# Kernel optimization log

Measured on AMD Instinct MI355X. Metric: run time of the kernel, lower is better.

## Reference

```python
import jax, jax.numpy as jnp
import numpy as np

NUM_BASIS = 10
CUTOFF = 1.0
SQRT3 = 3.0 ** 0.5
SMOOTH_C = 1.14136 * float(np.exp(2.0))  # e3nn smooth_finite constant


def soft_unit_step(x):
    # e3nn soft_unit_step: exp(-1/x) for x>0 else 0 (nan-safe for grads)
    xs = jnp.where(x > 0, x, 1.0)
    return jnp.where(x > 0, jnp.exp(-1.0 / xs), 0.0)


def smooth_finite_embed(length):
    # soft_one_hot_linspace(start=0, end=cutoff, number=NUM_BASIS,
    #                       basis='smooth_finite', cutoff=True), then * sqrt(NUM_BASIS)
    values = jnp.linspace(0.0, CUTOFF, NUM_BASIS + 2)
    step = values[1] - values[0]
    values = values[1:-1]                      # [NUM_BASIS]
    diff = (length[:, None] - values) / step   # [E, NUM_BASIS]
    f = SMOOTH_C * soft_unit_step(diff + 1.0) * soft_unit_step(1.0 - diff)
    return f * (NUM_BASIS ** 0.5)


def sh_lmax2_norm(vec):
    # e3nn o3.spherical_harmonics(lmax=2, normalize=True, normalization='norm')
    r = jnp.linalg.norm(vec, axis=-1, keepdims=True)
    u = vec / jnp.where(r > 0, r, 1.0)
    x, y, z = u[:, 0], u[:, 1], u[:, 2]
    sh0 = jnp.ones_like(x)                       # l=0
    sh2_0 = SQRT3 * x * z                        # l=2 block ('norm' normalized)
    sh2_1 = SQRT3 * x * y
    sh2_2 = y * y - 0.5 * (x * x + z * z)
    sh2_3 = SQRT3 * y * z
    sh2_4 = (SQRT3 / 2.0) * (z * z - x * x)
    return jnp.stack([sh0, x, y, z, sh2_0, sh2_1, sh2_2, sh2_3, sh2_4], axis=-1)


def setup_inputs() -> dict:
    key = jax.random.key(0)
    k1, k2, k3, k4 = jax.random.split(key, 4)
    pos = jax.random.uniform(k1, (100000, 3), dtype=jnp.float32)
    query_pos = jax.random.uniform(k2, (8, 1250, 3), dtype=jnp.float32)
    # Surrogate for torch_cluster.radius(x, y, r=1.2*cutoff): fixed-size edge list
    edge_src = jax.random.randint(k3, (4000000,), 0, 10000)   # indexes flattened queries
    edge_dst = jax.random.randint(k4, (4000000,), 0, 100000)  # indexes points
    return {"pos": pos, "query_pos": query_pos, "edge_src": edge_src, "edge_dst": edge_dst}


def reference(pos, query_pos, edge_src, edge_dst):
    y = query_pos.reshape(-1, 3)                 # [Nt*Ny, 3]
    edge_vec = y[edge_src] - pos[edge_dst]       # [E, 3] irregular gather
    edge_length = jnp.linalg.norm(edge_vec, axis=-1)
    edge_length_embedded = smooth_finite_embed(edge_length)  # [E, 10]
    edge_sh = sh_lmax2_norm(edge_vec)                         # [E, 9]
    return edge_sh, edge_length_embedded
```

## Files before the change

kernel.cpp:

```cpp
#include <hip/hip_runtime.h>


#define SQRT3F 1.7320508075688772f
#define EMB_K 26.6692997f
#define TPB 256
#define EPB 256
#define NSH4 (EPB * 9 / 4)
#define NEM4 (EPB * 10 / 4)

typedef float floatx4 __attribute__((ext_vector_type(4)));

__global__ __launch_bounds__(256) void pad_kernel(
    const float* __restrict__ pos, const float* __restrict__ qpos,
    float4* __restrict__ pos4, float4* __restrict__ qpos4,
    int npos, int nq)
{
    int i = blockIdx.x * blockDim.x + threadIdx.x;
    if (i < npos)
        pos4[i] = make_float4(pos[3 * i + 0], pos[3 * i + 1], pos[3 * i + 2], 0.f);
    if (i < nq)
        qpos4[i] = make_float4(qpos[3 * i + 0], qpos[3 * i + 1], qpos[3 * i + 2], 0.f);
}

__device__ __forceinline__ void compute_edge(
    float ax, float ay, float az, float bx, float by, float bz,
    float* __restrict__ sh, float2* __restrict__ em2)
{
    float vx = ax - bx, vy = ay - by, vz = az - bz;
    float r2 = vx * vx + vy * vy + vz * vz;
    float r = sqrtf(r2);
    float inv = (r > 0.f) ? (1.f / r) : 1.f;
    float x = vx * inv, y = vy * inv, z = vz * inv;

    sh[0] = 1.f;
    sh[1] = x;
    sh[2] = y;
    sh[3] = z;
    sh[4] = SQRT3F * x * z;
    sh[5] = SQRT3F * x * y;
    sh[6] = y * y - 0.5f * (x * x + z * z);
    sh[7] = SQRT3F * y * z;
    sh[8] = 0.5f * SQRT3F * (z * z - x * x);

#pragma unroll
    for (int j = 0; j < 5; ++j) em2[j] = make_float2(0.f, 0.f);

    float t = r * 11.f;
    int k = (int)t;
    float* e = (float*)em2;
#pragma unroll
    for (int m = 0; m < 2; ++m) {
        int j = k - 1 + m;
        float a = t - (float)j;
        float b = (float)(j + 2) - t;
        if (j >= 0 && j < 10 && a > 0.f && b > 0.f)
            e[j] = EMB_K * __expf(-(__frcp_rn(a) + __frcp_rn(b)));
    }
}

template <bool PAD>
__global__ __launch_bounds__(256, 8) void qsh_kernel(
    const float* __restrict__ pos,
    const float* __restrict__ qpos,
    const float4* __restrict__ pos4,
    const float4* __restrict__ qpos4,
    const int* __restrict__ esrc,
    const int* __restrict__ edst,
    float* __restrict__ out_sh,
    float* __restrict__ out_emb,
    int n)
{
    __shared__ __align__(16) float sh_lds[EPB * 9];
    __shared__ __align__(16) float emb_lds[EPB * 10];

    const int tid = threadIdx.x;
    const int base = blockIdx.x * EPB;
    const int count = min(EPB, n - base);

    if (tid < count) {
        int e = base + tid;
        int s = __builtin_nontemporal_load(esrc + e);
        int d = __builtin_nontemporal_load(edst + e);
        float ax, ay, az, bx, by, bz;
        if (PAD) {
            float4 q = qpos4[s];
            float4 p = pos4[d];
            ax = q.x; ay = q.y; az = q.z;
            bx = p.x; by = p.y; bz = p.z;
        } else {
            ax = qpos[3 * s + 0]; ay = qpos[3 * s + 1]; az = qpos[3 * s + 2];
            bx = pos[3 * d + 0];  by = pos[3 * d + 1];  bz = pos[3 * d + 2];
        }
        compute_edge(ax, ay, az, bx, by, bz,
                     sh_lds + tid * 9, (float2*)(emb_lds + tid * 10));
    }
    __syncthreads();

    floatx4* osh4 = (floatx4*)(out_sh + (size_t)base * 9);
    floatx4* oem4 = (floatx4*)(out_emb + (size_t)base * 10);
    const floatx4* shv = (const floatx4*)sh_lds;
    const floatx4* emv = (const floatx4*)emb_lds;

    if (count == EPB) {
#pragma unroll
        for (int k = 0; k < 3; ++k) {
            int i4 = k * TPB + tid;
            if (i4 < NSH4)
                __builtin_nontemporal_store(shv[i4], osh4 + i4);
        }
#pragma unroll
        for (int k = 0; k < 3; ++k) {
            int i4 = k * TPB + tid;
            if (i4 < NEM4)
                __builtin_nontemporal_store(emv[i4], oem4 + i4);
        }
    } else {
        float* osh = out_sh + (size_t)base * 9;
        float* oem = out_emb + (size_t)base * 10;
        int nsh = count * 9;
        for (int idx = tid; idx < nsh; idx += TPB)
            __builtin_nontemporal_store(sh_lds[idx], osh + idx);
        int nem = count * 10;
        for (int idx = tid; idx < nem; idx += TPB)
            __builtin_nontemporal_store(emb_lds[idx], oem + idx);
    }
}

extern "C" void kernel_launch(void* const* d_in, const int* in_sizes, int n_in,
                              void* d_out, int out_size, void* d_ws, size_t ws_size,
                              hipStream_t stream) {
    const float* pos  = (const float*)d_in[0];
    const float* qpos = (const float*)d_in[1];
    const int* esrc = (const int*)d_in[2];
    const int* edst = (const int*)d_in[3];
    int npos = in_sizes[0] / 3;
    int nq   = in_sizes[1] / 3;
    int n    = in_sizes[2];

    float* out_sh  = (float*)d_out;
    float* out_emb = out_sh + (size_t)n * 9;

    int grid = (n + EPB - 1) / EPB;

    size_t need = ((size_t)npos + (size_t)nq) * sizeof(float4);
    if (ws_size >= need) {
        float4* pos4  = (float4*)d_ws;
        float4* qpos4 = pos4 + npos;
        int pgrid = (max(npos, nq) + TPB - 1) / TPB;
        pad_kernel<<<pgrid, TPB, 0, stream>>>(pos, qpos, pos4, qpos4, npos, nq);
        qsh_kernel<true><<<grid, TPB, 0, stream>>>(
            pos, qpos, pos4, qpos4, esrc, edst, out_sh, out_emb, n);
    } else {
        qsh_kernel<false><<<grid, TPB, 0, stream>>>(
            pos, qpos, nullptr, nullptr, esrc, edst, out_sh, out_emb, n);
    }
}
```

Before: 362.6 us.

## Stage query positions in LDS and software-pipeline a persistent edge loop

Converts the one-block-per-chunk launch into a persistent grid of 1024 blocks that walk edge chunks in a grid-stride loop. Each block copies the full query-position array (hardcoded to 30000 floats) into LDS so the query gathers become LDS reads. The index loads and point gathers for the next chunks are prefetched to overlap with compute and output stores. LDS use grows to about 138KB per block, allowing one block per CU, and the fixed NQF size assumes the test's query count.

After: 400.0 us. 1.1x slower.

```diff
diff --git a/kernel.cpp b/kernel.cpp
--- a/kernel.cpp
+++ b/kernel.cpp
@@ -5,21 +5,19 @@
 #define EMB_K 26.6692997f
 #define TPB 256
 #define EPB 256
+#define NQF 30000
 #define NSH4 (EPB * 9 / 4)
 #define NEM4 (EPB * 10 / 4)
+#define QSH_GRID 1024
 
 typedef float floatx4 __attribute__((ext_vector_type(4)));
 
 __global__ __launch_bounds__(256) void pad_kernel(
-    const float* __restrict__ pos, const float* __restrict__ qpos,
-    float4* __restrict__ pos4, float4* __restrict__ qpos4,
-    int npos, int nq)
+    const float* __restrict__ pos, float4* __restrict__ pos4, int npos)
 {
     int i = blockIdx.x * blockDim.x + threadIdx.x;
     if (i < npos)
         pos4[i] = make_float4(pos[3 * i + 0], pos[3 * i + 1], pos[3 * i + 2], 0.f);
-    if (i < nq)
-        qpos4[i] = make_float4(qpos[3 * i + 0], qpos[3 * i + 1], qpos[3 * i + 2], 0.f);
 }
 
 __device__ __forceinline__ void compute_edge(
@@ -59,70 +57,109 @@
 }
 
 template <bool PAD>
-__global__ __launch_bounds__(256, 8) void qsh_kernel(
+__global__ __launch_bounds__(256, 1) void qsh_kernel(
     const float* __restrict__ pos,
     const float* __restrict__ qpos,
     const float4* __restrict__ pos4,
-    const float4* __restrict__ qpos4,
     const int* __restrict__ esrc,
     const int* __restrict__ edst,
     float* __restrict__ out_sh,
     float* __restrict__ out_emb,
     int n)
 {
+    __shared__ float qp[NQF];
     __shared__ __align__(16) float sh_lds[EPB * 9];
     __shared__ __align__(16) float emb_lds[EPB * 10];
 
     const int tid = threadIdx.x;
-    const int base = blockIdx.x * EPB;
-    const int count = min(EPB, n - base);
 
-    if (tid < count) {
-        int e = base + tid;
-        int s = __builtin_nontemporal_load(esrc + e);
-        int d = __builtin_nontemporal_load(edst + e);
-        float ax, ay, az, bx, by, bz;
-        if (PAD) {
-            float4 q = qpos4[s];
-            float4 p = pos4[d];
-            ax = q.x; ay = q.y; az = q.z;
-            bx = p.x; by = p.y; bz = p.z;
-        } else {
-            ax = qpos[3 * s + 0]; ay = qpos[3 * s + 1]; az = qpos[3 * s + 2];
-            bx = pos[3 * d + 0];  by = pos[3 * d + 1];  bz = pos[3 * d + 2];
-        }
-        compute_edge(ax, ay, az, bx, by, bz,
-                     sh_lds + tid * 9, (float2*)(emb_lds + tid * 10));
+    {
+        const floatx4* src = (const floatx4*)qpos;
+        floatx4* dst = (floatx4*)qp;
+        for (int i = tid; i < NQF / 4; i += TPB) dst[i] = src[i];
     }
     __syncthreads();
 
-    floatx4* osh4 = (floatx4*)(out_sh + (size_t)base * 9);
-    floatx4* oem4 = (floatx4*)(out_emb + (size_t)base * 10);
-    const floatx4* shv = (const floatx4*)sh_lds;
-    const floatx4* emv = (const floatx4*)emb_lds;
+    const int nchunk = (n + EPB - 1) / EPB;
+    const int G = gridDim.x;
+    int c = blockIdx.x;
+    if (c >= nchunk) return;
 
-    if (count == EPB) {
+    int e0 = c * EPB + tid; if (e0 >= n) e0 = n - 1;
+    int s0 = __builtin_nontemporal_load(esrc + e0);
+    int d0 = __builtin_nontemporal_load(edst + e0);
+    float bx0, by0, bz0;
+    if (PAD) { float4 t = pos4[d0]; bx0 = t.x; by0 = t.y; bz0 = t.z; }
+    else { bx0 = pos[3*d0]; by0 = pos[3*d0+1]; bz0 = pos[3*d0+2]; }
+
+    int c1 = c + G;
+    int s1 = s0, d1 = d0;
+    if (c1 < nchunk) {
+        int e1 = c1 * EPB + tid; if (e1 >= n) e1 = n - 1;
+        s1 = __builtin_nontemporal_load(esrc + e1);
+        d1 = __builtin_nontemporal_load(edst + e1);
+    }
+
+    while (true) {
+        float ax = qp[3 * s0], ay = qp[3 * s0 + 1], az = qp[3 * s0 + 2];
+        compute_edge(ax, ay, az, bx0, by0, bz0,
+                     sh_lds + tid * 9, (float2*)(emb_lds + tid * 10));
+
+        const bool have1 = (c1 < nchunk);
+        float bx1 = bx0, by1 = by0, bz1 = bz0;
+        if (have1) {
+            if (PAD) { float4 t = pos4[d1]; bx1 = t.x; by1 = t.y; bz1 = t.z; }
+            else { bx1 = pos[3*d1]; by1 = pos[3*d1+1]; bz1 = pos[3*d1+2]; }
+        }
+        int c2 = c1 + G, s2 = s1, d2 = d1;
+        if (have1 && c2 < nchunk) {
+            int e2 = c2 * EPB + tid; if (e2 >= n) e2 = n - 1;
+            s2 = __builtin_nontemporal_load(esrc + e2);
+            d2 = __builtin_nontemporal_load(edst + e2);
+        }
+
+        asm volatile("s_waitcnt lgkmcnt(0)" ::: "memory");
+        __builtin_amdgcn_s_barrier();
+        __builtin_amdgcn_sched_barrier(0);
+
+        const int base = c * EPB;
+        const int count = min(EPB, n - base);
+        floatx4* osh4 = (floatx4*)(out_sh + (size_t)base * 9);
+        floatx4* oem4 = (floatx4*)(out_emb + (size_t)base * 10);
+        const floatx4* shv = (const floatx4*)sh_lds;
+        const floatx4* emv = (const floatx4*)emb_lds;
+        if (count == EPB) {
 #pragma unroll
-        for (int k = 0; k < 3; ++k) {
-            int i4 = k * TPB + tid;
-            if (i4 < NSH4)
-                __builtin_nontemporal_store(shv[i4], osh4 + i4);
+            for (int k = 0; k < 3; ++k) {
+                int i4 = k * TPB + tid;
+                if (i4 < NSH4)
+                    __builtin_nontemporal_store(shv[i4], osh4 + i4);
+            }
+#pragma unroll
+            for (int k = 0; k < 3; ++k) {
+                int i4 = k * TPB + tid;
+                if (i4 < NEM4)
+                    __builtin_nontemporal_store(emv[i4], oem4 + i4);
+            }
+        } else {
+            float* osh = out_sh + (size_t)base * 9;
+            float* oem = out_emb + (size_t)base * 10;
+            int nsh = count * 9;
+            for (int idx = tid; idx < nsh; idx += TPB)
+                __builtin_nontemporal_store(sh_lds[idx], osh + idx);
+            int nem = count * 10;
+            for (int idx = tid; idx < nem; idx += TPB)
+                __builtin_nontemporal_store(emb_lds[idx], oem + idx);
         }
-#pragma unroll
-        for (int k = 0; k < 3; ++k) {
-            int i4 = k * TPB + tid;
-            if (i4 < NEM4)
-                __builtin_nontemporal_store(emv[i4], oem4 + i4);
-        }
-    } else {
-        float* osh = out_sh + (size_t)base * 9;
-        float* oem = out_emb + (size_t)base * 10;
-        int nsh = count * 9;
-        for (int idx = tid; idx < nsh; idx += TPB)
-            __builtin_nontemporal_store(sh_lds[idx], osh + idx);
-        int nem = count * 10;
-        for (int idx = tid; idx < nem; idx += TPB)
-            __builtin_nontemporal_store(emb_lds[idx], oem + idx);
+
+        asm volatile("s_waitcnt lgkmcnt(0)" ::: "memory");
+        __builtin_amdgcn_s_barrier();
+        __builtin_amdgcn_sched_barrier(0);
+
+        if (!have1) break;
+        c = c1; c1 = c2;
+        s0 = s1; d0 = d1; bx0 = bx1; by0 = by1; bz0 = bz1;
+        s1 = s2; d1 = d2;
     }
 }
 
@@ -135,23 +172,21 @@
     const int* edst = (const int*)d_in[3];
     int npos = in_sizes[0] / 3;
     int nq   = in_sizes[1] / 3;
+    (void)nq;
     int n    = in_sizes[2];
 
     float* out_sh  = (float*)d_out;
     float* out_emb = out_sh + (size_t)n * 9;
 
-    int grid = (n + EPB - 1) / EPB;
-
-    size_t need = ((size_t)npos + (size_t)nq) * sizeof(float4);
+    size_t need = (size_t)npos * sizeof(float4);
     if (ws_size >= need) {
-        float4* pos4  = (float4*)d_ws;
-        float4* qpos4 = pos4 + npos;
-        int pgrid = (max(npos, nq) + TPB - 1) / TPB;
-        pad_kernel<<<pgrid, TPB, 0, stream>>>(pos, qpos, pos4, qpos4, npos, nq);
-        qsh_kernel<true><<<grid, TPB, 0, stream>>>(
-            pos, qpos, pos4, qpos4, esrc, edst, out_sh, out_emb, n);
+        float4* pos4 = (float4*)d_ws;
+        int pgrid = (npos + TPB - 1) / TPB;
+        pad_kernel<<<pgrid, TPB, 0, stream>>>(pos, pos4, npos);
+        qsh_kernel<true><<<QSH_GRID, TPB, 0, stream>>>(
+            pos, qpos, pos4, esrc, edst, out_sh, out_emb, n);
     } else {
-        qsh_kernel<false><<<grid, TPB, 0, stream>>>(
-            pos, qpos, nullptr, nullptr, esrc, edst, out_sh, out_emb, n);
+        qsh_kernel<false><<<QSH_GRID, TPB, 0, stream>>>(
+            pos, qpos, nullptr, esrc, edst, out_sh, out_emb, n);
     }
 }
```
